# Performance work log

Hardware: AMD Instinct MI355X
Metric: run time of the kernel (lower is better)

The kernel has to match this reference:

```python
import jax, jax.numpy as jnp
import numpy as np

N, C, H, W = 4, 256, 64, 64
K, G, PAD, STRIDE, DIL = 3, 8, 1, 1, 1
GC = C // G      # channels per group
P = K * K        # sampling points per group
HIN, WIN = H + 2 * PAD, W + 2 * PAD
BN_EPS = 1e-5
LN_EPS = 1e-5


def setup_inputs():
    key = jax.random.key(0)
    ks = jax.random.split(key, 8)
    f32 = jnp.float32
    return {
        "x": jax.random.normal(ks[0], (N, C, H, W), dtype=f32),
        "w_in": jax.random.normal(ks[1], (C, C), dtype=f32) * 0.05,
        "b_in": jnp.zeros((C,), f32),
        "w_dw": jax.random.normal(ks[2], (C, 1, K, K), dtype=f32) * 0.1,
        "b_dw": jnp.zeros((C,), f32),
        "ln_g": jnp.ones((C,), f32), "ln_b": jnp.zeros((C,), f32),
        "w_off": jax.random.normal(ks[3], (C, G * P * 2), dtype=f32) * 0.01,
        "b_off": jax.random.normal(ks[4], (G * P * 2,), dtype=f32) * 0.01,
        "w_mask": jax.random.normal(ks[5], (C, G * P), dtype=f32) * 0.01,
        "b_mask": jnp.zeros((G * P,), f32),
        "w_out": jax.random.normal(ks[6], (C, C), dtype=f32) * 0.05,
        "b_out": jnp.zeros((C,), f32),
        "bn_g": jnp.ones((C,), f32), "bn_b": jnp.zeros((C,), f32),
        "bn_mean": jnp.zeros((C,), f32), "bn_var": jnp.ones((C,), f32),
    }


def _bilinear(img, grid):
    # img: (B, Cc, Hh, Ww); grid: (B, S, P, 2) normalized to [-1,1],
    # matches F.grid_sample(mode='bilinear', padding_mode='zeros', align_corners=False)
    B, Cc, Hh, Ww = img.shape
    gx = (grid[..., 0] + 1.0) * 0.5 * Ww - 0.5
    gy = (grid[..., 1] + 1.0) * 0.5 * Hh - 0.5
    x0 = jnp.floor(gx)
    y0 = jnp.floor(gy)
    wx = gx - x0
    wy = gy - y0
    flat = img.reshape(B, Cc, Hh * Ww)

    def tap(xi, yi, wgt):
        valid = (xi >= 0) & (xi <= Ww - 1) & (yi >= 0) & (yi <= Hh - 1)
        idx = (jnp.clip(yi, 0, Hh - 1) * Ww + jnp.clip(xi, 0, Ww - 1)).astype(jnp.int32)
        v = jax.vmap(lambda im, ix: im[:, ix])(flat, idx)   # (B, Cc, S, P)
        return v * (wgt * valid.astype(img.dtype))[:, None]

    return (tap(x0, y0, (1 - wx) * (1 - wy)) + tap(x0 + 1, y0, wx * (1 - wy))
            + tap(x0, y0 + 1, (1 - wx) * wy) + tap(x0 + 1, y0 + 1, wx * wy))


def _forward(x, w_in, b_in, w_dw, b_dw, ln_g, ln_b, w_off, b_off,
             w_mask, b_mask, w_out, b_out, bn_g, bn_b, bn_mean, bn_var):
    xl = jnp.transpose(x, (0, 2, 3, 1))                      # (N,H,W,C) channels-last
    x_proj = xl @ w_in + b_in                                # input_proj
    # depthwise conv + LayerNorm + GELU feature branch for offset/mask prediction
    dw = jax.lax.conv_general_dilated(
        x, w_dw, (1, 1), ((PAD, PAD), (PAD, PAD)),
        feature_group_count=C, dimension_numbers=("NCHW", "OIHW", "NCHW"))
    dw = jnp.transpose(dw + b_dw[None, :, None, None], (0, 2, 3, 1))
    mu = dw.mean(-1, keepdims=True)
    var = ((dw - mu) ** 2).mean(-1, keepdims=True)
    dw = (dw - mu) * jax.lax.rsqrt(var + LN_EPS) * ln_g + ln_b
    x1 = jax.nn.gelu(dw, approximate=False)
    offset = x1 @ w_off + b_off                              # (N,H,W,G*P*2)
    mask = jax.nn.softmax((x1 @ w_mask + b_mask).reshape(N, H, W, G, P), axis=-1)
    # reference points + dilation kernel grid, normalized to padded input, (x,y) order
    ry = ((DIL * (K - 1)) // 2 + 0.5 + jnp.arange(H, dtype=x.dtype) * STRIDE) / HIN
    rx = ((DIL * (K - 1)) // 2 + 0.5 + jnp.arange(W, dtype=x.dtype) * STRIDE) / WIN
    ref = jnp.stack(jnp.broadcast_arrays(rx[None, :], ry[:, None]), axis=-1)  # (H,W,2)
    px = (jnp.arange(K, dtype=x.dtype) * DIL - (DIL * (K - 1)) // 2) / WIN
    py = (jnp.arange(K, dtype=x.dtype) * DIL - (DIL * (K - 1)) // 2) / HIN
    gx, gy = jnp.meshgrid(px, py, indexing="ij")             # kw-major flattening as in DCNv3
    kgrid = jnp.stack([gx, gy], -1).reshape(P, 2)
    norm = jnp.array([WIN, HIN], dtype=x.dtype)
    loc = (ref[None, :, :, None, None, :] + kgrid[None, None, None, None, :, :]
           + offset.reshape(N, H, W, G, P, 2) / norm)        # (N,H,W,G,P,2), offset_scale=1
    sgrid = 2.0 * loc - 1.0
    # group-split padded value tensor and deformable sampling
    xp = jnp.pad(x_proj, ((0, 0), (PAD, PAD), (PAD, PAD), (0, 0)))
    img = jnp.transpose(xp, (0, 3, 1, 2)).reshape(N * G, GC, HIN, WIN)
    sg = jnp.transpose(sgrid.reshape(N, H * W, G, P, 2), (0, 2, 1, 3, 4)).reshape(N * G, H * W, P, 2)
    sampled = _bilinear(img, sg)                             # (N*G, GC, H*W, P)
    m = jnp.transpose(mask.reshape(N, H * W, G, P), (0, 2, 1, 3)).reshape(N * G, 1, H * W, P)
    agg = (sampled * m).sum(-1)                              # (N*G, GC, H*W)
    y = jnp.transpose(agg.reshape(N, C, H * W), (0, 2, 1)).reshape(N, H, W, C)
    y = y @ w_out + b_out                                    # output_proj
    y = jnp.transpose(y, (0, 3, 1, 2))                       # back to NCHW
    y = (y - bn_mean[None, :, None, None]) * jax.lax.rsqrt(bn_var + BN_EPS)[None, :, None, None]
    y = y * bn_g[None, :, None, None] + bn_b[None, :, None, None]
    return y * jax.nn.sigmoid(y)                             # SiLU (Conv.default_act)


def reference(x, w_in, b_in, w_dw, b_dw, ln_g, ln_b, w_off, b_off,
              w_mask, b_mask, w_out, b_out, bn_g, bn_b, bn_mean, bn_var):
    return _forward(x, w_in, b_in, w_dw, b_dw, ln_g, ln_b, w_off, b_off,
                    w_mask, b_mask, w_out, b_out, bn_g, bn_b, bn_mean, bn_var)
```

## Files before the change

kernel.cpp:

```cpp
#include <hip/hip_runtime.h>
#include <math.h>

#define NB   4
#define CCH  256
#define HH   64
#define WW   64
#define GG   8
#define GCH  32
#define PP   9
#define HIN  66
#define WIN  66
#define HWSZ 4096
#define NPIX 16384

#define XP_ELEMS  (NB*HIN*WIN*CCH)
#define X1_ELEMS  (NPIX*CCH)
#define OFF_ELEMS (NPIX*144)
#define MSK_ELEMS (NPIX*72)
#define AGG_ELEMS (NPIX*CCH)

typedef __attribute__((ext_vector_type(8))) short bf16x8;
typedef __attribute__((ext_vector_type(4))) float f32x4;

__device__ __forceinline__ unsigned short f2bf(float f) {
    unsigned int u = __float_as_uint(f);
    unsigned int r = (u + 0x7FFFu + ((u >> 16) & 1u)) >> 16;
    return (unsigned short)r;
}
__device__ __forceinline__ float bf2f(unsigned short s) {
    unsigned int u = ((unsigned int)s) << 16;
    return __uint_as_float(u);
}

#define AK 40

__global__ __launch_bounds__(64) void k_zero_ring(float* __restrict__ xp)
{
    int b = blockIdx.x;
    int n = b / 260;
    int rp = b % 260;
    int h, w;
    if (rp < 66)       { h = 0;        w = rp; }
    else if (rp < 132) { h = 65;       w = rp - 66; }
    else if (rp < 196) { h = rp - 131; w = 0; }
    else               { h = rp - 195; w = 65; }
    float4 z = make_float4(0.f, 0.f, 0.f, 0.f);
    *(float4*)&xp[(((size_t)n * HIN + h) * WIN + w) * CCH + threadIdx.x * 4] = z;
}

__global__ __launch_bounds__(256) void k_gemm_in(
    const float* __restrict__ x, const float* __restrict__ w_in,
    const float* __restrict__ b_in, float* __restrict__ xp)
{
    __shared__ short As[128 * AK];
    __shared__ short Ws[64 * AK];

    const int m0  = blockIdx.x * 128;
    const int co0 = blockIdx.y * 64;
    const int tid = threadIdx.x;
    const int n   = m0 >> 12;
    const int hw0 = m0 & 4095;

    const int wave = tid >> 6;
    const int lane = tid & 63;
    const int r16  = lane & 15;
    const int quad = lane >> 4;
    const int mw   = wave * 32;

    const float* xa = x + (size_t)n * CCH * HWSZ + hw0;

    f32x4 acc[2][4];
#pragma unroll
    for (int i = 0; i < 2; i++)
#pragma unroll
        for (int j = 0; j < 4; j++) acc[i][j] = (f32x4){0.f, 0.f, 0.f, 0.f};

    for (int k0 = 0; k0 < CCH; k0 += 32) {
#pragma unroll
        for (int l = 0; l < 16; l++) {
            int idx = tid + l * 256;
            int kk = idx >> 7, m = idx & 127;
            As[m * AK + kk] = (short)f2bf(xa[(size_t)(k0 + kk) * HWSZ + m]);
        }
#pragma unroll
        for (int l = 0; l < 8; l++) {
            int idx = tid + l * 256;
            int nn = idx & 63, kk = idx >> 6;
            Ws[nn * AK + kk] = (short)f2bf(w_in[(size_t)(k0 + kk) * CCH + co0 + nn]);
        }
        __syncthreads();

        bf16x8 a0 = *(const bf16x8*)&As[(mw + r16) * AK + quad * 8];
        bf16x8 a1 = *(const bf16x8*)&As[(mw + 16 + r16) * AK + quad * 8];
#pragma unroll
        for (int nt = 0; nt < 4; nt++) {
            bf16x8 bfr = *(const bf16x8*)&Ws[(nt * 16 + r16) * AK + quad * 8];
            acc[0][nt] = __builtin_amdgcn_mfma_f32_16x16x32_bf16(a0, bfr, acc[0][nt], 0, 0, 0);
            acc[1][nt] = __builtin_amdgcn_mfma_f32_16x16x32_bf16(a1, bfr, acc[1][nt], 0, 0, 0);
        }
        __syncthreads();
    }

#pragma unroll
    for (int nt = 0; nt < 4; nt++) {
        int co = co0 + nt * 16 + r16;
        float bias = b_in[co];
#pragma unroll
        for (int mt = 0; mt < 2; mt++) {
            int mbase = mw + mt * 16 + quad * 4;
#pragma unroll
            for (int r = 0; r < 4; r++) {
                int hw = hw0 + mbase + r;
                int h = hw >> 6, w = hw & 63;
                xp[(((size_t)n * HIN + (h + 1)) * WIN + (w + 1)) * CCH + co] =
                    acc[mt][nt][r] + bias;
            }
        }
    }
}

#define SDW_STRIDE 258
__global__ __launch_bounds__(512) void k_dw_ln_gelu(
    const float* __restrict__ x, const float* __restrict__ w_dw,
    const float* __restrict__ b_dw, const float* __restrict__ ln_g,
    const float* __restrict__ ln_b, float* __restrict__ x1)
{
    __shared__ unsigned short sdw[64 * SDW_STRIDE];
    __shared__ float r1s[8][64];
    __shared__ float r2s[8][64];
    __shared__ float mu_s[64];
    __shared__ float rs_s[64];

    const int h = blockIdx.x;
    const int n = blockIdx.y;
    const int tid = threadIdx.x;
    const int wave = tid >> 6;
    const int lane = tid & 63;

    const float* xn = x + (size_t)n * CCH * HWSZ;
    const bool h0ok = (h > 0);
    const bool h2ok = (h < HH - 1);

    float s1 = 0.f, s2 = 0.f;

#pragma unroll 4
    for (int it = 0; it < 32; it++) {
        const int c = it * 8 + wave;
        const float* xc = xn + (size_t)c * HWSZ + h * WW + lane;
        float v0 = h0ok ? xc[-WW] : 0.f;
        float v1 = xc[0];
        float v2 = h2ok ? xc[WW] : 0.f;

        const float* wk = w_dw + c * 9;
        float acc = b_dw[c];

        float l0 = __shfl_up(v0, 1);  if (lane == 0)  l0 = 0.f;
        float r0 = __shfl_down(v0, 1); if (lane == 63) r0 = 0.f;
        acc += wk[0] * l0 + wk[1] * v0 + wk[2] * r0;

        float l1 = __shfl_up(v1, 1);  if (lane == 0)  l1 = 0.f;
        float r1 = __shfl_down(v1, 1); if (lane == 63) r1 = 0.f;
        acc += wk[3] * l1 + wk[4] * v1 + wk[5] * r1;

        float l2 = __shfl_up(v2, 1);  if (lane == 0)  l2 = 0.f;
        float r2 = __shfl_down(v2, 1); if (lane == 63) r2 = 0.f;
        acc += wk[6] * l2 + wk[7] * v2 + wk[8] * r2;

        s1 += acc;
        s2 += acc * acc;
        sdw[lane * SDW_STRIDE + c] = f2bf(acc);
    }

    r1s[wave][lane] = s1;
    r2s[wave][lane] = s2;
    __syncthreads();

    if (tid < 64) {
        float a1 = 0.f, a2 = 0.f;
#pragma unroll
        for (int q = 0; q < 8; q++) { a1 += r1s[q][tid]; a2 += r2s[q][tid]; }
        float mu = a1 * (1.0f / 256.0f);
        float var = a2 * (1.0f / 256.0f) - mu * mu;
        mu_s[tid] = mu;
        rs_s[tid] = rsqrtf(var + 1e-5f);
    }
    __syncthreads();

    const int c0 = (tid & 63) * 4;
    const int wq = tid >> 6;
    float g4[4], b4[4];
#pragma unroll
    for (int i = 0; i < 4; i++) { g4[i] = ln_g[c0 + i]; b4[i] = ln_b[c0 + i]; }

    float* x1p = x1 + (((size_t)n * HH + h) * WW) * CCH + c0;
#pragma unroll
    for (int pass = 0; pass < 8; pass++) {
        int w = wq + pass * 8;
        float mu = mu_s[w], rs = rs_s[w];
        const unsigned short* row = &sdw[w * SDW_STRIDE + c0];
        float tmp[4];
#pragma unroll
        for (int i = 0; i < 4; i++) {
            float v = (bf2f(row[i]) - mu) * rs * g4[i] + b4[i];
            tmp[i] = 0.5f * v * (1.0f + erff(v * 0.70710678118654752f));
        }
        *(float4*)&x1p[(size_t)w * CCH] = make_float4(tmp[0], tmp[1], tmp[2], tmp[3]);
    }
}

__global__ __launch_bounds__(256) void k_gemm_offmask(
    const float* __restrict__ x1, const float* __restrict__ w_off,
    const float* __restrict__ b_off, const float* __restrict__ w_mask,
    const float* __restrict__ b_mask, float* __restrict__ off,
    float* __restrict__ msk)
{
    __shared__ short As[128 * AK];
    __shared__ short Ws[64 * AK];

    const int m0  = blockIdx.x * 128;
    const int co0 = blockIdx.y * 64;
    const int tid = threadIdx.x;

    const int wave = tid >> 6;
    const int lane = tid & 63;
    const int r16  = lane & 15;
    const int quad = lane >> 4;
    const int mw   = wave * 32;

    f32x4 acc[2][4];
#pragma unroll
    for (int i = 0; i < 2; i++)
#pragma unroll
        for (int j = 0; j < 4; j++) acc[i][j] = (f32x4){0.f, 0.f, 0.f, 0.f};

    for (int k0 = 0; k0 < CCH; k0 += 32) {
#pragma unroll
        for (int l = 0; l < 4; l++) {
            int idx = tid + l * 256;
            int m = idx >> 3, kq = idx & 7;
            float4 v = *(const float4*)&x1[(size_t)(m0 + m) * CCH + k0 + kq * 4];
            short4 s;
            s.x = (short)f2bf(v.x); s.y = (short)f2bf(v.y);
            s.z = (short)f2bf(v.z); s.w = (short)f2bf(v.w);
            *(short4*)&As[m * AK + kq * 4] = s;
        }
#pragma unroll
        for (int l = 0; l < 8; l++) {
            int idx = tid + l * 256;
            int nn = idx & 63, kk = idx >> 6;
            int col = co0 + nn;
            float wv = 0.f;
            if (col < 144)      wv = w_off[(size_t)(k0 + kk) * 144 + col];
            else if (col < 216) wv = w_mask[(size_t)(k0 + kk) * 72 + col - 144];
            Ws[nn * AK + kk] = (short)f2bf(wv);
        }
        __syncthreads();

        bf16x8 a0 = *(const bf16x8*)&As[(mw + r16) * AK + quad * 8];
        bf16x8 a1 = *(const bf16x8*)&As[(mw + 16 + r16) * AK + quad * 8];
#pragma unroll
        for (int nt = 0; nt < 4; nt++) {
            bf16x8 bfr = *(const bf16x8*)&Ws[(nt * 16 + r16) * AK + quad * 8];
            acc[0][nt] = __builtin_amdgcn_mfma_f32_16x16x32_bf16(a0, bfr, acc[0][nt], 0, 0, 0);
            acc[1][nt] = __builtin_amdgcn_mfma_f32_16x16x32_bf16(a1, bfr, acc[1][nt], 0, 0, 0);
        }
        __syncthreads();
    }

#pragma unroll
    for (int nt = 0; nt < 4; nt++) {
        int col = co0 + nt * 16 + r16;
        if (col >= 216) continue;
        float bias = (col < 144) ? b_off[col] : b_mask[col - 144];
#pragma unroll
        for (int mt = 0; mt < 2; mt++) {
            int mbase = m0 + mw + mt * 16 + quad * 4;
#pragma unroll
            for (int r = 0; r < 4; r++) {
                int p = mbase + r;
                float v = acc[mt][nt][r] + bias;
                if (col < 144) off[(size_t)p * 144 + col] = v;
                else           msk[(size_t)p * 72 + col - 144] = v;
            }
        }
    }
}

__global__ __launch_bounds__(256) void k_sample_agg(
    const float* __restrict__ xp, const float* __restrict__ off,
    const float* __restrict__ msk, float* __restrict__ agg)
{
    __shared__ float  sm[288];
    __shared__ int2   tco[288];
    __shared__ float4 twt[288];

    const int tid = threadIdx.x;
    const int s0 = blockIdx.x * 4;

    if (tid < 32) {
        const int pix = tid >> 3, g = tid & 7;
        const float* mskp = msk + (size_t)(s0 + pix) * 72 + g * 9;
        float e[9];
        float mx = -1e30f;
#pragma unroll
        for (int p = 0; p < PP; p++) { e[p] = mskp[p]; mx = fmaxf(mx, e[p]); }
        float sum = 0.f;
#pragma unroll
        for (int p = 0; p < PP; p++) { e[p] = __expf(e[p] - mx); sum += e[p]; }
        float rs = 1.0f / sum;
#pragma unroll
        for (int p = 0; p < PP; p++) sm[tid * 9 + p] = e[p] * rs;
    }
    __syncthreads();

    for (int idx = tid; idx < 288; idx += 256) {
        int pix = idx / 72;
        int rem = idx - pix * 72;
        int g = rem / 9;
        int p = rem - g * 9;
        int s = s0 + pix;
        int hw = s & 4095;
        int h = hw >> 6, w = hw & 63;
        const float* offp = off + (size_t)s * 144 + g * 18 + p * 2;
        float ox = offp[0], oy = offp[1];
        int i = p / 3, j = p - i * 3;
        float fx = (float)(w + i) + ox;
        float fy = (float)(h + j) + oy;
        float x0f = floorf(fx), y0f = floorf(fy);
        int x0 = (int)x0f, y0 = (int)y0f;
        float wx = fx - x0f, wy = fy - y0f;
        float m = sm[idx];
        float w00 = (1.f - wx) * (1.f - wy) * m;
        float w10 = wx * (1.f - wy) * m;
        float w01 = (1.f - wx) * wy * m;
        float w11 = wx * wy * m;
        int x1c = x0 + 1, y1c = y0 + 1;
        if (!((x0  >= 0) && (x0  < WIN))) { w00 = 0.f; w01 = 0.f; }
        if (!((x1c >= 0) && (x1c < WIN))) { w10 = 0.f; w11 = 0.f; }
        if (!((y0  >= 0) && (y0  < HIN))) { w00 = 0.f; w10 = 0.f; }
        if (!((y1c >= 0) && (y1c < HIN))) { w01 = 0.f; w11 = 0.f; }
        int cx0 = min(max(x0, 0), WIN - 1), cx1 = min(max(x1c, 0), WIN - 1);
        int cy0 = min(max(y0, 0), HIN - 1), cy1 = min(max(y1c, 0), HIN - 1);
        tco[idx] = make_int2(cx0 | (cx1 << 16), cy0 | (cy1 << 16));
        twt[idx] = make_float4(w00, w10, w01, w11);
    }
    __syncthreads();

    const int pix = tid >> 6;
    const int lane = tid & 63;
    const int g = lane >> 3, c4 = lane & 7;
    const int s = s0 + pix;
    const int n = s >> 12;
    const float* base = xp + (size_t)n * HIN * WIN * CCH + g * GCH + c4 * 4;
    const int tbase = pix * 72 + g * 9;

    float ax = 0.f, ay = 0.f, az = 0.f, aw = 0.f;
#pragma unroll
    for (int p = 0; p < PP; p++) {
        int2 cc = tco[tbase + p];
        float4 wt = twt[tbase + p];
        int cx0 = cc.x & 0xFFFF, cx1 = cc.x >> 16;
        int cy0 = cc.y & 0xFFFF, cy1 = cc.y >> 16;
        const float* r0 = base + (size_t)(cy0 * WIN) * CCH;
        const float* r1 = base + (size_t)(cy1 * WIN) * CCH;
        float4 v00 = *(const float4*)&r0[(size_t)cx0 * CCH];
        float4 v10 = *(const float4*)&r0[(size_t)cx1 * CCH];
        float4 v01 = *(const float4*)&r1[(size_t)cx0 * CCH];
        float4 v11 = *(const float4*)&r1[(size_t)cx1 * CCH];
        ax += wt.x * v00.x + wt.y * v10.x + wt.z * v01.x + wt.w * v11.x;
        ay += wt.x * v00.y + wt.y * v10.y + wt.z * v01.y + wt.w * v11.y;
        az += wt.x * v00.z + wt.y * v10.z + wt.z * v01.z + wt.w * v11.z;
        aw += wt.x * v00.w + wt.y * v10.w + wt.z * v01.w + wt.w * v11.w;
    }

    *(float4*)&agg[(size_t)s * CCH + g * GCH + c4 * 4] = make_float4(ax, ay, az, aw);
}

__global__ __launch_bounds__(256) void k_gemm_out(
    const float* __restrict__ agg, const float* __restrict__ w_out,
    const float* __restrict__ b_out, const float* __restrict__ bn_g,
    const float* __restrict__ bn_b, const float* __restrict__ bn_mean,
    const float* __restrict__ bn_var, float* __restrict__ out)
{
    __shared__ short As[128 * AK];
    __shared__ short Ws[64 * AK];

    const int m0  = blockIdx.x * 128;
    const int co0 = blockIdx.y * 64;
    const int tid = threadIdx.x;
    const int n   = m0 >> 12;
    const int hw0 = m0 & 4095;

    const int wave = tid >> 6;
    const int lane = tid & 63;
    const int r16  = lane & 15;
    const int quad = lane >> 4;
    const int mw   = wave * 32;

    f32x4 acc[2][4];
#pragma unroll
    for (int i = 0; i < 2; i++)
#pragma unroll
        for (int j = 0; j < 4; j++) acc[i][j] = (f32x4){0.f, 0.f, 0.f, 0.f};

    for (int k0 = 0; k0 < CCH; k0 += 32) {
#pragma unroll
        for (int l = 0; l < 4; l++) {
            int idx = tid + l * 256;
            int m = idx >> 3, kq = idx & 7;
            float4 v = *(const float4*)&agg[(size_t)(m0 + m) * CCH + k0 + kq * 4];
            short4 s;
            s.x = (short)f2bf(v.x); s.y = (short)f2bf(v.y);
            s.z = (short)f2bf(v.z); s.w = (short)f2bf(v.w);
            *(short4*)&As[m * AK + kq * 4] = s;
        }
#pragma unroll
        for (int l = 0; l < 8; l++) {
            int idx = tid + l * 256;
            int nn = idx & 63, kk = idx >> 6;
            Ws[nn * AK + kk] = (short)f2bf(w_out[(size_t)(k0 + kk) * CCH + co0 + nn]);
        }
        __syncthreads();

        bf16x8 a0 = *(const bf16x8*)&As[(mw + r16) * AK + quad * 8];
        bf16x8 a1 = *(const bf16x8*)&As[(mw + 16 + r16) * AK + quad * 8];
#pragma unroll
        for (int nt = 0; nt < 4; nt++) {
            bf16x8 bfr = *(const bf16x8*)&Ws[(nt * 16 + r16) * AK + quad * 8];
            acc[0][nt] = __builtin_amdgcn_mfma_f32_16x16x32_bf16(a0, bfr, acc[0][nt], 0, 0, 0);
            acc[1][nt] = __builtin_amdgcn_mfma_f32_16x16x32_bf16(a1, bfr, acc[1][nt], 0, 0, 0);
        }
        __syncthreads();
    }

#pragma unroll
    for (int nt = 0; nt < 4; nt++) {
        int co = co0 + nt * 16 + r16;
        float mean = bn_mean[co];
        float rstd = rsqrtf(bn_var[co] + 1e-5f);
        float gg = bn_g[co], bb = bn_b[co], bo = b_out[co];
#pragma unroll
        for (int mt = 0; mt < 2; mt++) {
            int hwb = hw0 + mw + mt * 16 + quad * 4;
            float tmp[4];
#pragma unroll
            for (int r = 0; r < 4; r++) {
                float y = acc[mt][nt][r] + bo;
                float yh = (y - mean) * rstd * gg + bb;
                tmp[r] = yh / (1.0f + __expf(-yh));
            }
            float4 v = make_float4(tmp[0], tmp[1], tmp[2], tmp[3]);
            *(float4*)&out[((size_t)n * CCH + co) * HWSZ + hwb] = v;
        }
    }
}

extern "C" void kernel_launch(void* const* d_in, const int* in_sizes, int n_in,
                              void* d_out, int out_size, void* d_ws, size_t ws_size,
                              hipStream_t stream)
{
    const float* x       = (const float*)d_in[0];
    const float* w_in    = (const float*)d_in[1];
    const float* b_in    = (const float*)d_in[2];
    const float* w_dw    = (const float*)d_in[3];
    const float* b_dw    = (const float*)d_in[4];
    const float* ln_g    = (const float*)d_in[5];
    const float* ln_b    = (const float*)d_in[6];
    const float* w_off   = (const float*)d_in[7];
    const float* b_off   = (const float*)d_in[8];
    const float* w_mask  = (const float*)d_in[9];
    const float* b_mask  = (const float*)d_in[10];
    const float* w_out   = (const float*)d_in[11];
    const float* b_out   = (const float*)d_in[12];
    const float* bn_g    = (const float*)d_in[13];
    const float* bn_b    = (const float*)d_in[14];
    const float* bn_mean = (const float*)d_in[15];
    const float* bn_var  = (const float*)d_in[16];
    float* out = (float*)d_out;

    float* ws  = (float*)d_ws;
    float* xp  = ws;
    float* x1  = xp + XP_ELEMS;
    float* off = x1 + X1_ELEMS;
    float* msk = off + OFF_ELEMS;
    float* agg = msk + MSK_ELEMS;

    k_zero_ring<<<dim3(1040), 64, 0, stream>>>(xp);
    k_gemm_in<<<dim3(128, 4), 256, 0, stream>>>(x, w_in, b_in, xp);
    k_dw_ln_gelu<<<dim3(64, 4), 512, 0, stream>>>(x, w_dw, b_dw, ln_g, ln_b, x1);
    k_gemm_offmask<<<dim3(128, 4), 256, 0, stream>>>(x1, w_off, b_off, w_mask, b_mask, off, msk);
    k_sample_agg<<<dim3(4096), 256, 0, stream>>>(xp, off, msk, agg);
    k_gemm_out<<<dim3(128, 4), 256, 0, stream>>>(agg, w_out, b_out, bn_g, bn_b, bn_mean, bn_var, out);
}
```

Before: 219.8 us.

## Store intermediate activations xp, x1, agg in bf16 instead of fp32

```diff
diff --git a/kernel.cpp b/kernel.cpp
--- a/kernel.cpp
+++ b/kernel.cpp
@@ -15,9 +15,9 @@
 
 #define XP_ELEMS  (NB*HIN*WIN*CCH)
 #define X1_ELEMS  (NPIX*CCH)
+#define AGG_ELEMS (NPIX*CCH)
 #define OFF_ELEMS (NPIX*144)
 #define MSK_ELEMS (NPIX*72)
-#define AGG_ELEMS (NPIX*CCH)
 
 typedef __attribute__((ext_vector_type(8))) short bf16x8;
 typedef __attribute__((ext_vector_type(4))) float f32x4;
@@ -28,13 +28,15 @@
     return (unsigned short)r;
 }
 __device__ __forceinline__ float bf2f(unsigned short s) {
-    unsigned int u = ((unsigned int)s) << 16;
-    return __uint_as_float(u);
+    return __uint_as_float(((unsigned int)s) << 16);
+}
+__device__ __forceinline__ unsigned int f2bf_pk(float lo, float hi) {
+    return (unsigned int)f2bf(lo) | ((unsigned int)f2bf(hi) << 16);
 }
 
 #define AK 40
 
-__global__ __launch_bounds__(64) void k_zero_ring(float* __restrict__ xp)
+__global__ __launch_bounds__(64) void k_zero_ring(unsigned short* __restrict__ xp)
 {
     int b = blockIdx.x;
     int n = b / 260;
@@ -44,13 +46,13 @@
     else if (rp < 132) { h = 65;       w = rp - 66; }
     else if (rp < 196) { h = rp - 131; w = 0; }
     else               { h = rp - 195; w = 65; }
-    float4 z = make_float4(0.f, 0.f, 0.f, 0.f);
-    *(float4*)&xp[(((size_t)n * HIN + h) * WIN + w) * CCH + threadIdx.x * 4] = z;
+    uint2 z = make_uint2(0u, 0u);
+    *(uint2*)&xp[(((size_t)n * HIN + h) * WIN + w) * CCH + threadIdx.x * 4] = z;
 }
 
 __global__ __launch_bounds__(256) void k_gemm_in(
     const float* __restrict__ x, const float* __restrict__ w_in,
-    const float* __restrict__ b_in, float* __restrict__ xp)
+    const float* __restrict__ b_in, unsigned short* __restrict__ xp)
 {
     __shared__ short As[128 * AK];
     __shared__ short Ws[64 * AK];
@@ -77,16 +79,20 @@
 
     for (int k0 = 0; k0 < CCH; k0 += 32) {
 #pragma unroll
-        for (int l = 0; l < 16; l++) {
-            int idx = tid + l * 256;
-            int kk = idx >> 7, m = idx & 127;
-            As[m * AK + kk] = (short)f2bf(xa[(size_t)(k0 + kk) * HWSZ + m]);
-        }
-#pragma unroll
         for (int l = 0; l < 8; l++) {
             int idx = tid + l * 256;
-            int nn = idx & 63, kk = idx >> 6;
-            Ws[nn * AK + kk] = (short)f2bf(w_in[(size_t)(k0 + kk) * CCH + co0 + nn]);
+            int m = idx & 127, kp = idx >> 7;
+            float v0 = xa[(size_t)(k0 + 2 * kp) * HWSZ + m];
+            float v1 = xa[(size_t)(k0 + 2 * kp + 1) * HWSZ + m];
+            ((unsigned int*)As)[(m * AK) / 2 + kp] = f2bf_pk(v0, v1);
+        }
+#pragma unroll
+        for (int l = 0; l < 4; l++) {
+            int idx = tid + l * 256;
+            int nn = idx & 63, kp = idx >> 6;
+            float v0 = w_in[(size_t)(k0 + 2 * kp) * CCH + co0 + nn];
+            float v1 = w_in[(size_t)(k0 + 2 * kp + 1) * CCH + co0 + nn];
+            ((unsigned int*)Ws)[(nn * AK) / 2 + kp] = f2bf_pk(v0, v1);
         }
         __syncthreads();
 
@@ -113,7 +119,7 @@
                 int hw = hw0 + mbase + r;
                 int h = hw >> 6, w = hw & 63;
                 xp[(((size_t)n * HIN + (h + 1)) * WIN + (w + 1)) * CCH + co] =
-                    acc[mt][nt][r] + bias;
+                    f2bf(acc[mt][nt][r] + bias);
             }
         }
     }
@@ -123,7 +129,7 @@
 __global__ __launch_bounds__(512) void k_dw_ln_gelu(
     const float* __restrict__ x, const float* __restrict__ w_dw,
     const float* __restrict__ b_dw, const float* __restrict__ ln_g,
-    const float* __restrict__ ln_b, float* __restrict__ x1)
+    const float* __restrict__ ln_b, unsigned short* __restrict__ x1)
 {
     __shared__ unsigned short sdw[64 * SDW_STRIDE];
     __shared__ float r1s[8][64];
@@ -192,24 +198,25 @@
 #pragma unroll
     for (int i = 0; i < 4; i++) { g4[i] = ln_g[c0 + i]; b4[i] = ln_b[c0 + i]; }
 
-    float* x1p = x1 + (((size_t)n * HH + h) * WW) * CCH + c0;
+    unsigned short* x1p = x1 + (((size_t)n * HH + h) * WW) * CCH + c0;
 #pragma unroll
     for (int pass = 0; pass < 8; pass++) {
         int w = wq + pass * 8;
         float mu = mu_s[w], rs = rs_s[w];
         const unsigned short* row = &sdw[w * SDW_STRIDE + c0];
-        float tmp[4];
+        unsigned short tmp[4];
 #pragma unroll
         for (int i = 0; i < 4; i++) {
             float v = (bf2f(row[i]) - mu) * rs * g4[i] + b4[i];
-            tmp[i] = 0.5f * v * (1.0f + erff(v * 0.70710678118654752f));
-        }
-        *(float4*)&x1p[(size_t)w * CCH] = make_float4(tmp[0], tmp[1], tmp[2], tmp[3]);
+            tmp[i] = f2bf(0.5f * v * (1.0f + erff(v * 0.70710678118654752f)));
+        }
+        ushort4 o; o.x = tmp[0]; o.y = tmp[1]; o.z = tmp[2]; o.w = tmp[3];
+        *(ushort4*)&x1p[(size_t)w * CCH] = o;
     }
 }
 
 __global__ __launch_bounds__(256) void k_gemm_offmask(
-    const float* __restrict__ x1, const float* __restrict__ w_off,
+    const unsigned short* __restrict__ x1, const float* __restrict__ w_off,
     const float* __restrict__ b_off, const float* __restrict__ w_mask,
     const float* __restrict__ b_mask, float* __restrict__ off,
     float* __restrict__ msk)
@@ -235,24 +242,26 @@
 
     for (int k0 = 0; k0 < CCH; k0 += 32) {
 #pragma unroll
+        for (int l = 0; l < 2; l++) {
+            int idx = tid + l * 256;
+            int m = idx >> 2, kq = idx & 3;
+            uint4 v = *(const uint4*)&x1[(size_t)(m0 + m) * CCH + k0 + kq * 8];
+            *(uint4*)&As[m * AK + kq * 8] = v;
+        }
+#pragma unroll
         for (int l = 0; l < 4; l++) {
             int idx = tid + l * 256;
-            int m = idx >> 3, kq = idx & 7;
-            float4 v = *(const float4*)&x1[(size_t)(m0 + m) * CCH + k0 + kq * 4];
-            short4 s;
-            s.x = (short)f2bf(v.x); s.y = (short)f2bf(v.y);
-            s.z = (short)f2bf(v.z); s.w = (short)f2bf(v.w);
-            *(short4*)&As[m * AK + kq * 4] = s;
-        }
-#pragma unroll
-        for (int l = 0; l < 8; l++) {
-            int idx = tid + l * 256;
-            int nn = idx & 63, kk = idx >> 6;
+            int nn = idx & 63, kp = idx >> 6;
             int col = co0 + nn;
-            float wv = 0.f;
-            if (col < 144)      wv = w_off[(size_t)(k0 + kk) * 144 + col];
-            else if (col < 216) wv = w_mask[(size_t)(k0 + kk) * 72 + col - 144];
-            Ws[nn * AK + kk] = (short)f2bf(wv);
+            float v0 = 0.f, v1 = 0.f;
+            if (col < 144) {
+                v0 = w_off[(size_t)(k0 + 2 * kp) * 144 + col];
+                v1 = w_off[(size_t)(k0 + 2 * kp + 1) * 144 + col];
+            } else if (col < 216) {
+                v0 = w_mask[(size_t)(k0 + 2 * kp) * 72 + col - 144];
+                v1 = w_mask[(size_t)(k0 + 2 * kp + 1) * 72 + col - 144];
+            }
+            ((unsigned int*)Ws)[(nn * AK) / 2 + kp] = f2bf_pk(v0, v1);
         }
         __syncthreads();
 
@@ -287,8 +296,8 @@
 }
 
 __global__ __launch_bounds__(256) void k_sample_agg(
-    const float* __restrict__ xp, const float* __restrict__ off,
-    const float* __restrict__ msk, float* __restrict__ agg)
+    const unsigned short* __restrict__ xp, const float* __restrict__ off,
+    const float* __restrict__ msk, unsigned short* __restrict__ agg)
 {
     __shared__ float  sm[288];
     __shared__ int2   tco[288];
@@ -351,7 +360,7 @@
     const int g = lane >> 3, c4 = lane & 7;
     const int s = s0 + pix;
     const int n = s >> 12;
-    const float* base = xp + (size_t)n * HIN * WIN * CCH + g * GCH + c4 * 4;
+    const unsigned short* base = xp + (size_t)n * HIN * WIN * CCH + g * GCH + c4 * 4;
     const int tbase = pix * 72 + g * 9;
 
     float ax = 0.f, ay = 0.f, az = 0.f, aw = 0.f;
@@ -361,23 +370,24 @@
         float4 wt = twt[tbase + p];
         int cx0 = cc.x & 0xFFFF, cx1 = cc.x >> 16;
         int cy0 = cc.y & 0xFFFF, cy1 = cc.y >> 16;
-        const float* r0 = base + (size_t)(cy0 * WIN) * CCH;
-        const float* r1 = base + (size_t)(cy1 * WIN) * CCH;
-        float4 v00 = *(const float4*)&r0[(size_t)cx0 * CCH];
-        float4 v10 = *(const float4*)&r0[(size_t)cx1 * CCH];
-        float4 v01 = *(const float4*)&r1[(size_t)cx0 * CCH];
-        float4 v11 = *(const float4*)&r1[(size_t)cx1 * CCH];
-        ax += wt.x * v00.x + wt.y * v10.x + wt.z * v01.x + wt.w * v11.x;
-        ay += wt.x * v00.y + wt.y * v10.y + wt.z * v01.y + wt.w * v11.y;
-        az += wt.x * v00.z + wt.y * v10.z + wt.z * v01.z + wt.w * v11.z;
-        aw += wt.x * v00.w + wt.y * v10.w + wt.z * v01.w + wt.w * v11.w;
-    }
-
-    *(float4*)&agg[(size_t)s * CCH + g * GCH + c4 * 4] = make_float4(ax, ay, az, aw);
+        const unsigned short* r0 = base + (size_t)(cy0 * WIN) * CCH;
+        const unsigned short* r1 = base + (size_t)(cy1 * WIN) * CCH;
+        ushort4 v00 = *(const ushort4*)&r0[(size_t)cx0 * CCH];
+        ushort4 v10 = *(const ushort4*)&r0[(size_t)cx1 * CCH];
+        ushort4 v01 = *(const ushort4*)&r1[(size_t)cx0 * CCH];
+        ushort4 v11 = *(const ushort4*)&r1[(size_t)cx1 * CCH];
+        ax += wt.x * bf2f(v00.x) + wt.y * bf2f(v10.x) + wt.z * bf2f(v01.x) + wt.w * bf2f(v11.x);
+        ay += wt.x * bf2f(v00.y) + wt.y * bf2f(v10.y) + wt.z * bf2f(v01.y) + wt.w * bf2f(v11.y);
+        az += wt.x * bf2f(v00.z) + wt.y * bf2f(v10.z) + wt.z * bf2f(v01.z) + wt.w * bf2f(v11.z);
+        aw += wt.x * bf2f(v00.w) + wt.y * bf2f(v10.w) + wt.z * bf2f(v01.w) + wt.w * bf2f(v11.w);
+    }
+
+    ushort4 o; o.x = f2bf(ax); o.y = f2bf(ay); o.z = f2bf(az); o.w = f2bf(aw);
+    *(ushort4*)&agg[(size_t)s * CCH + g * GCH + c4 * 4] = o;
 }
 
 __global__ __launch_bounds__(256) void k_gemm_out(
-    const float* __restrict__ agg, const float* __restrict__ w_out,
+    const unsigned short* __restrict__ agg, const float* __restrict__ w_out,
     const float* __restrict__ b_out, const float* __restrict__ bn_g,
     const float* __restrict__ bn_b, const float* __restrict__ bn_mean,
     const float* __restrict__ bn_var, float* __restrict__ out)
@@ -405,20 +415,19 @@
 
     for (int k0 = 0; k0 < CCH; k0 += 32) {
 #pragma unroll
+        for (int l = 0; l < 2; l++) {
+            int idx = tid + l * 256;
+            int m = idx >> 2, kq = idx & 3;
+            uint4 v = *(const uint4*)&agg[(size_t)(m0 + m) * CCH + k0 + kq * 8];
+            *(uint4*)&As[m * AK + kq * 8] = v;
+        }
+#pragma unroll
         for (int l = 0; l < 4; l++) {
             int idx = tid + l * 256;
-            int m = idx >> 3, kq = idx & 7;
-            float4 v = *(const float4*)&agg[(size_t)(m0 + m) * CCH + k0 + kq * 4];
-            short4 s;
-            s.x = (short)f2bf(v.x); s.y = (short)f2bf(v.y);
-            s.z = (short)f2bf(v.z); s.w = (short)f2bf(v.w);
-            *(short4*)&As[m * AK + kq * 4] = s;
-        }
-#pragma unroll
-        for (int l = 0; l < 8; l++) {
-            int idx = tid + l * 256;
-            int nn = idx & 63, kk = idx >> 6;
-            Ws[nn * AK + kk] = (short)f2bf(w_out[(size_t)(k0 + kk) * CCH + co0 + nn]);
+            int nn = idx & 63, kp = idx >> 6;
+            float v0 = w_out[(size_t)(k0 + 2 * kp) * CCH + co0 + nn];
+            float v1 = w_out[(size_t)(k0 + 2 * kp + 1) * CCH + co0 + nn];
+            ((unsigned int*)Ws)[(nn * AK) / 2 + kp] = f2bf_pk(v0, v1);
         }
         __syncthreads();
 
@@ -478,12 +487,11 @@
     const float* bn_var  = (const float*)d_in[16];
     float* out = (float*)d_out;
 
-    float* ws  = (float*)d_ws;
-    float* xp  = ws;
-    float* x1  = xp + XP_ELEMS;
-    float* off = x1 + X1_ELEMS;
+    unsigned short* xp  = (unsigned short*)d_ws;
+    unsigned short* x1  = xp + XP_ELEMS;
+    unsigned short* agg = x1 + X1_ELEMS;
+    float* off = (float*)(agg + AGG_ELEMS);
     float* msk = off + OFF_ELEMS;
-    float* agg = msk + MSK_ELEMS;
 
     k_zero_ring<<<dim3(1040), 64, 0, stream>>>(xp);
     k_gemm_in<<<dim3(128, 4), 256, 0, stream>>>(x, w_in, b_in, xp);
```

Measured after the change: 181.5 us. 1.21x faster.
